# Kernel tuning notes

Measured on AMD Instinct MI355X. Metric: run time of the kernel, lower is better.

Reference implementation:

```python
import jax, jax.numpy as jnp
import numpy as np

N = 50000      # nodes
E = 800000     # edges
C = 128        # dim_feat / channels
D = 256        # dim_dense
OUT = 2        # dim_out
L = 5          # num_layers - 1 GCN2Conv layers
ALPHA = 0.1    # main_param -> GCN2Conv alpha; theta=None -> beta=1.0
SLOPE = 0.01   # LeakyReLU default negative slope


def setup_inputs() -> dict:
    key = jax.random.key(0)
    ks = jax.random.split(key, 6)
    x = jax.random.normal(ks[0], (N, C), jnp.float32)
    edge_index = jax.random.randint(ks[1], (2, E), 0, N, jnp.int32)
    conv_weights = jax.random.normal(ks[2], (L, C, C), jnp.float32) * (1.0 / np.sqrt(C))
    w_dense = jax.random.normal(ks[3], (C, D), jnp.float32) * (1.0 / np.sqrt(C))
    b_dense = jnp.zeros((D,), jnp.float32)
    w_out = jax.random.normal(ks[4], (D, OUT), jnp.float32) * (1.0 / np.sqrt(D))
    b_out = jnp.zeros((OUT,), jnp.float32)
    return dict(x=x, edge_index=edge_index, conv_weights=conv_weights,
                w_dense=w_dense, b_dense=b_dense, w_out=w_out, b_out=b_out)


def _gcn_norm(edge_index, num_nodes):
    """Symmetric gcn_norm with self-loops: returns row, col, D^-1/2 * D^-1/2 edge weights."""
    loop = jnp.arange(num_nodes, dtype=edge_index.dtype)
    row = jnp.concatenate([edge_index[0], loop])  # sources
    col = jnp.concatenate([edge_index[1], loop])  # targets (aggregation index)
    ones = jnp.ones(row.shape[0], jnp.float32)
    deg = jax.ops.segment_sum(ones, col, num_segments=num_nodes)
    dinv = jnp.where(deg > 0, jax.lax.rsqrt(jnp.maximum(deg, 1e-12)), 0.0)
    return row, col, dinv[row] * dinv[col]


def reference(x, edge_index, conv_weights, w_dense, b_dense, w_out, b_out):
    num_nodes = x.shape[0]
    row, col, norm = _gcn_norm(edge_index, num_nodes)
    x0 = x
    for l in range(conv_weights.shape[0]):
        # propagate: h[i] = sum_{j->i} norm * x[j]   (gather -> scatter-add)
        h = jax.ops.segment_sum(norm[:, None] * x[row], col, num_segments=num_nodes)
        # GCN2Conv with shared_weights=True, beta=1 (theta=None): out = ((1-a)h + a*x0) @ W
        out = (1.0 - ALPHA) * h + ALPHA * x0
        x = jax.nn.leaky_relu(out @ conv_weights[l], negative_slope=SLOPE)
    x = x @ w_dense + b_dense
    return x @ w_out + b_out
```

## Files before the change

kernel.cpp:

```cpp
#include <hip/hip_runtime.h>
#include <hip/hip_fp16.h>

#define C 128
#define NOUT 2
#define ALPHA 0.1f
#define SLOPE 0.01f
#define ZP 136

typedef _Float16 half4v __attribute__((ext_vector_type(4)));
typedef float float4v __attribute__((ext_vector_type(4)));


__global__ void count_kernel(const int* __restrict__ col, int* __restrict__ cnt, int E) {
    int e = blockIdx.x * 256 + threadIdx.x;
    if (e < E) atomicAdd(&cnt[col[e]], 1);
}

__global__ __launch_bounds__(1024) void scanA_kernel(const int* __restrict__ cnt,
                                                     int* __restrict__ offs,
                                                     int* __restrict__ bsum,
                                                     float* __restrict__ dinv, int n) {
    __shared__ int wsum[16];
    int t = threadIdx.x, lane = t & 63, wv = t >> 6;
    int i = blockIdx.x * 1024 + t;
    int v = (i < n) ? cnt[i] : 0;
    if (i < n) dinv[i] = rsqrtf((float)(v + 1));
    int sc = v;
    #pragma unroll
    for (int d = 1; d < 64; d <<= 1) {
        int u = __shfl_up(sc, d);
        if (lane >= d) sc += u;
    }
    if (lane == 63) wsum[wv] = sc;
    __syncthreads();
    int woff = 0;
    #pragma unroll
    for (int j = 0; j < 16; ++j) woff += (j < wv) ? wsum[j] : 0;
    if (i < n) offs[i] = woff + sc - v;
    if (t == 0) {
        int tot = 0;
        #pragma unroll
        for (int j = 0; j < 16; ++j) tot += wsum[j];
        bsum[blockIdx.x] = tot;
    }
}

__global__ __launch_bounds__(1024) void scanB_kernel(const int* __restrict__ bsum,
                                                     int* __restrict__ bbase, int nb) {
    __shared__ int wsum[16];
    int t = threadIdx.x, lane = t & 63, wv = t >> 6;
    int v = (t < nb) ? bsum[t] : 0;
    int sc = v;
    #pragma unroll
    for (int d = 1; d < 64; d <<= 1) {
        int u = __shfl_up(sc, d);
        if (lane >= d) sc += u;
    }
    if (lane == 63) wsum[wv] = sc;
    __syncthreads();
    int woff = 0;
    #pragma unroll
    for (int j = 0; j < 16; ++j) woff += (j < wv) ? wsum[j] : 0;
    if (t < nb) bbase[t] = woff + sc - v;
}

__global__ void scanC_kernel(int* __restrict__ offs, int* __restrict__ cursor,
                             const int* __restrict__ bbase, int n, int E) {
    int i = blockIdx.x * 256 + threadIdx.x;
    if (i < n) {
        int o = offs[i] + bbase[i >> 10];
        offs[i] = o;
        cursor[i] = o;
    }
    if (i == n) offs[n] = E;
}

__global__ void fill_kernel(const int* __restrict__ row, const int* __restrict__ col,
                            const float* __restrict__ dinv, int* __restrict__ cursor,
                            unsigned* __restrict__ csr, int E) {
    int base = blockIdx.x * 1024 + threadIdx.x;
    int r[4], c[4];
    bool v[4];
    #pragma unroll
    for (int j = 0; j < 4; ++j) {
        int e = base + j * 256;
        v[j] = e < E;
        r[j] = v[j] ? row[e] : 0;
        c[j] = v[j] ? col[e] : 0;
    }
    float nr[4];
    #pragma unroll
    for (int j = 0; j < 4; ++j) nr[j] = dinv[r[j]] * dinv[c[j]];
    int pos[4];
    #pragma unroll
    for (int j = 0; j < 4; ++j)
        pos[j] = v[j] ? atomicAdd(&cursor[c[j]], 1) : 0;
    #pragma unroll
    for (int j = 0; j < 4; ++j) {
        if (v[j]) {
            union { __half h; unsigned short u; } nh;
            nh.h = __float2half_rn(nr[j]);
            csr[pos[j]] = ((unsigned)r[j] << 16) | (unsigned)nh.u;
        }
    }
}

__global__ __launch_bounds__(256) void convert_kernel(const float* __restrict__ x,
                                                      __half* __restrict__ xh, int n) {
    int g = blockIdx.x * 256 + threadIdx.x;
    if (g >= n * 32) return;
    float4 v = ((const float4*)x)[g];
    union { __half2 h; unsigned u; } a, b;
    a.h = __float22half2_rn(make_float2(v.x, v.y));
    b.h = __float22half2_rn(make_float2(v.z, v.w));
    ((uint2*)xh)[g] = make_uint2(a.u, b.u);
}

__global__ void wtc_kernel(const float* __restrict__ W, _Float16* __restrict__ WT, int total) {
    int idx = blockIdx.x * 256 + threadIdx.x;
    if (idx >= total) return;
    int l = idx >> 14, rem = idx & 16383;
    int nrow = rem >> 7, kk = rem & 127;
    WT[idx] = (_Float16)W[(l << 14) + kk * C + nrow];
}

__global__ void wdc_kernel(const float* __restrict__ wd, _Float16* __restrict__ WDT) {
    int idx = blockIdx.x * 256 + threadIdx.x;
    if (idx >= 256 * C) return;
    int nrow = idx >> 7, kk = idx & 127;
    WDT[idx] = (_Float16)wd[kk * 256 + nrow];
}

__device__ __forceinline__ void accum8(float* a, uint4 q, float w) {
    union { unsigned u; __half2 h; } c;
    float2 f;
    c.u = q.x; f = __half22float2(c.h); a[0] += w * f.x; a[1] += w * f.y;
    c.u = q.y; f = __half22float2(c.h); a[2] += w * f.x; a[3] += w * f.y;
    c.u = q.z; f = __half22float2(c.h); a[4] += w * f.x; a[5] += w * f.y;
    c.u = q.w; f = __half22float2(c.h); a[6] += w * f.x; a[7] += w * f.y;
}

__device__ __forceinline__ uint4 pack8(const float* a) {
    union { __half2 h; unsigned u; } c0, c1, c2, c3;
    c0.h = __float22half2_rn(make_float2(a[0], a[1]));
    c1.h = __float22half2_rn(make_float2(a[2], a[3]));
    c2.h = __float22half2_rn(make_float2(a[4], a[5]));
    c3.h = __float22half2_rn(make_float2(a[6], a[7]));
    return make_uint4(c0.u, c1.u, c2.u, c3.u);
}

__device__ __forceinline__ float norm_of(unsigned m) {
    union { unsigned short u; __half h; } nh;
    nh.u = (unsigned short)(m & 0xffffu);
    return __half2float(nh.h);
}

__global__ __launch_bounds__(256) void agg_kernel(
    const __half* __restrict__ xc, const __half* __restrict__ x0h,
    const int* __restrict__ offs, const unsigned* __restrict__ csr,
    const float* __restrict__ dinv, __half* __restrict__ z, int n)
{
    int node = blockIdx.x * 4 + (threadIdx.x >> 6);
    if (node >= n) return;
    int lane = threadIdx.x & 63;
    int eslot = lane >> 4, cg = lane & 15;
    const uint4* x4 = (const uint4*)xc;
    float a0[8] = {}, a1[8] = {}, a2[8] = {}, a3[8] = {};
    int beg = offs[node], end = offs[node + 1];
    int k = beg + eslot;
    for (; k + 12 < end; k += 16) {
        unsigned m0 = csr[k], m1 = csr[k + 4], m2 = csr[k + 8], m3 = csr[k + 12];
        uint4 q0 = x4[(size_t)(m0 >> 16) * 16 + cg];
        uint4 q1 = x4[(size_t)(m1 >> 16) * 16 + cg];
        uint4 q2 = x4[(size_t)(m2 >> 16) * 16 + cg];
        uint4 q3 = x4[(size_t)(m3 >> 16) * 16 + cg];
        accum8(a0, q0, norm_of(m0));
        accum8(a1, q1, norm_of(m1));
        accum8(a2, q2, norm_of(m2));
        accum8(a3, q3, norm_of(m3));
    }
    for (; k < end; k += 4) {
        unsigned m = csr[k];
        uint4 q = x4[(size_t)(m >> 16) * 16 + cg];
        accum8(a0, q, norm_of(m));
    }
    #pragma unroll
    for (int j = 0; j < 8; ++j) a0[j] += a1[j] + a2[j] + a3[j];
    #pragma unroll
    for (int j = 0; j < 8; ++j) {
        a0[j] += __shfl_xor(a0[j], 16);
        a0[j] += __shfl_xor(a0[j], 32);
    }
    if (eslot == 0) {
        float di = dinv[node], sw = di * di;
        uint4 qs = x4[(size_t)node * 16 + cg];
        accum8(a0, qs, sw);
        uint4 q0x = ((const uint4*)x0h)[(size_t)node * 16 + cg];
        float xr[8] = {};
        accum8(xr, q0x, 1.f);
        float zz[8];
        #pragma unroll
        for (int j = 0; j < 8; ++j) zz[j] = (1.f - ALPHA) * a0[j] + ALPHA * xr[j];
        ((uint4*)z)[(size_t)node * 16 + cg] = pack8(zz);
    }
}

__global__ __launch_bounds__(256) void layer_mfma(
    const __half* __restrict__ zin, const _Float16* __restrict__ WT,
    __half* __restrict__ xn, int n)
{
    __shared__ _Float16 zl[64 * ZP];
    __shared__ _Float16 ol[64 * ZP];
    int i0 = blockIdx.x * 64;
    int t = threadIdx.x;
    int w = t >> 6, lane = t & 63;
    int c = lane & 15, g = lane >> 4;

    const uint4* z4 = (const uint4*)zin;
    for (int p = t; p < 64 * 16; p += 256) {
        int r = p >> 4, c8 = p & 15;
        uint4 zv = make_uint4(0, 0, 0, 0);
        if (i0 + r < n) zv = z4[(size_t)(i0 + r) * 16 + c8];
        *(uint4*)&zl[r * ZP + c8 * 8] = zv;
    }

    half4v bf[8][2];
    #pragma unroll
    for (int kb = 0; kb < 8; ++kb)
        #pragma unroll
        for (int nt = 0; nt < 2; ++nt)
            bf[kb][nt] = *(const half4v*)&WT[((w * 2 + nt) * 16 + c) * C + kb * 16 + 4 * g];

    __syncthreads();

    #pragma unroll
    for (int m = 0; m < 4; ++m) {
        const _Float16* arow = &zl[(m * 16 + c) * ZP];
        half4v af[8];
        #pragma unroll
        for (int kb = 0; kb < 8; ++kb) af[kb] = *(const half4v*)&arow[kb * 16 + 4 * g];
        float4v acc0 = (float4v)0.f, acc1 = (float4v)0.f;
        #pragma unroll
        for (int kb = 0; kb < 8; ++kb) {
            acc0 = __builtin_amdgcn_mfma_f32_16x16x16f16(af[kb], bf[kb][0], acc0, 0, 0, 0);
            acc1 = __builtin_amdgcn_mfma_f32_16x16x16f16(af[kb], bf[kb][1], acc1, 0, 0, 0);
        }
        #pragma unroll
        for (int r = 0; r < 4; ++r) {
            float v0 = acc0[r]; v0 = v0 > 0.f ? v0 : SLOPE * v0;
            float v1 = acc1[r]; v1 = v1 > 0.f ? v1 : SLOPE * v1;
            ol[(m * 16 + 4 * g + r) * ZP + (w * 2 + 0) * 16 + c] = (_Float16)v0;
            ol[(m * 16 + 4 * g + r) * ZP + (w * 2 + 1) * 16 + c] = (_Float16)v1;
        }
    }
    __syncthreads();
    for (int p = t; p < 64 * 16; p += 256) {
        int r = p >> 4, c8 = p & 15;
        int node = i0 + r;
        if (node < n)
            ((uint4*)xn)[(size_t)node * 16 + c8] = *(uint4*)&ol[r * ZP + c8 * 8];
    }
}

__global__ __launch_bounds__(256) void dense_mfma(
    const __half* __restrict__ xin, const _Float16* __restrict__ WDT,
    const float* __restrict__ bd, const float* __restrict__ wo,
    const float* __restrict__ bo, float* __restrict__ out, int n)
{
    __shared__ _Float16 xl[64 * ZP];
    __shared__ float pp[64][4][2];
    int i0 = blockIdx.x * 64;
    int t = threadIdx.x;
    int w = t >> 6, lane = t & 63;
    int c = lane & 15, g = lane >> 4;

    const uint4* g4 = (const uint4*)xin;
    for (int p = t; p < 64 * 16; p += 256) {
        int r = p >> 4, c8 = p & 15;
        uint4 v = make_uint4(0, 0, 0, 0);
        if (i0 + r < n) v = g4[(size_t)(i0 + r) * 16 + c8];
        *(uint4*)&xl[r * ZP + c8 * 8] = v;
    }

    half4v bf[8][4];
    #pragma unroll
    for (int kb = 0; kb < 8; ++kb)
        #pragma unroll
        for (int nt = 0; nt < 4; ++nt)
            bf[kb][nt] = *(const half4v*)&WDT[((w * 4 + nt) * 16 + c) * C + kb * 16 + 4 * g];
    float bdv[4], wo0[4], wo1[4];
    #pragma unroll
    for (int nt = 0; nt < 4; ++nt) {
        int coln = (w * 4 + nt) * 16 + c;
        bdv[nt] = bd[coln];
        wo0[nt] = wo[coln * 2 + 0];
        wo1[nt] = wo[coln * 2 + 1];
    }

    __syncthreads();

    #pragma unroll
    for (int m = 0; m < 4; ++m) {
        const _Float16* arow = &xl[(m * 16 + c) * ZP];
        half4v af[8];
        #pragma unroll
        for (int kb = 0; kb < 8; ++kb) af[kb] = *(const half4v*)&arow[kb * 16 + 4 * g];
        float4v acc[4];
        #pragma unroll
        for (int nt = 0; nt < 4; ++nt) acc[nt] = (float4v)0.f;
        #pragma unroll
        for (int kb = 0; kb < 8; ++kb) {
            #pragma unroll
            for (int nt = 0; nt < 4; ++nt)
                acc[nt] = __builtin_amdgcn_mfma_f32_16x16x16f16(af[kb], bf[kb][nt], acc[nt], 0, 0, 0);
        }
        float p0[4] = {0.f, 0.f, 0.f, 0.f}, p1[4] = {0.f, 0.f, 0.f, 0.f};
        #pragma unroll
        for (int nt = 0; nt < 4; ++nt) {
            #pragma unroll
            for (int r = 0; r < 4; ++r) {
                float hv = acc[nt][r] + bdv[nt];
                p0[r] += hv * wo0[nt];
                p1[r] += hv * wo1[nt];
            }
        }
        #pragma unroll
        for (int ms = 1; ms <= 8; ms <<= 1) {
            #pragma unroll
            for (int r = 0; r < 4; ++r) {
                p0[r] += __shfl_xor(p0[r], ms);
                p1[r] += __shfl_xor(p1[r], ms);
            }
        }
        if (c == 0) {
            #pragma unroll
            for (int r = 0; r < 4; ++r) {
                pp[m * 16 + 4 * g + r][w][0] = p0[r];
                pp[m * 16 + 4 * g + r][w][1] = p1[r];
            }
        }
    }
    __syncthreads();
    if (t < 128) {
        int r = t >> 1, o = t & 1;
        int node = i0 + r;
        if (node < n) {
            float s = pp[r][0][o] + pp[r][1][o] + pp[r][2][o] + pp[r][3][o];
            out[(size_t)node * NOUT + o] = s + bo[o];
        }
    }
}

extern "C" void kernel_launch(void* const* d_in, const int* in_sizes, int n_in,
                              void* d_out, int out_size, void* d_ws, size_t ws_size,
                              hipStream_t stream) {
    const float* x0    = (const float*)d_in[0];
    const int*   ei    = (const int*)d_in[1];
    const float* convW = (const float*)d_in[2];
    const float* wd    = (const float*)d_in[3];
    const float* bd    = (const float*)d_in[4];
    const float* wo    = (const float*)d_in[5];
    const float* bo    = (const float*)d_in[6];
    float* out = (float*)d_out;

    int N = in_sizes[0] / C;
    int E = in_sizes[1] / 2;
    int L = in_sizes[2] / (C * C);
    const int* row = ei;
    const int* col = ei + E;
    int NB = (N + 1023) / 1024;

    char* p = (char*)d_ws;
    auto alloc = [&](size_t bytes) {
        char* r = p;
        p += (bytes + 255) & ~(size_t)255;
        return r;
    };
    int*      cnt    = (int*)alloc((size_t)N * 4);
    int*      offs   = (int*)alloc((size_t)(N + 1) * 4);
    int*      cursor = (int*)alloc((size_t)N * 4);
    int*      bsum   = (int*)alloc((size_t)NB * 4);
    int*      bbase  = (int*)alloc((size_t)NB * 4);
    unsigned* csr    = (unsigned*)alloc((size_t)E * 4);
    float*    dinv   = (float*)alloc((size_t)N * 4);
    __half*   x0h    = (__half*)alloc((size_t)N * C * 2);
    __half*   bufA   = (__half*)alloc((size_t)N * C * 2);
    __half*   zbuf   = (__half*)alloc((size_t)N * C * 2);
    _Float16* WT     = (_Float16*)alloc((size_t)L * C * C * 2);
    _Float16* WDT    = (_Float16*)alloc((size_t)256 * C * 2);

    hipMemsetAsync(cnt, 0, (size_t)N * 4, stream);
    count_kernel<<<(E + 255) / 256, 256, 0, stream>>>(col, cnt, E);
    scanA_kernel<<<NB, 1024, 0, stream>>>(cnt, offs, bsum, dinv, N);
    scanB_kernel<<<1, 1024, 0, stream>>>(bsum, bbase, NB);
    scanC_kernel<<<(N + 256) / 256, 256, 0, stream>>>(offs, cursor, bbase, N, E);
    fill_kernel<<<(E + 1023) / 1024, 256, 0, stream>>>(row, col, dinv, cursor, csr, E);
    convert_kernel<<<(N * 32 + 255) / 256, 256, 0, stream>>>(x0, x0h, N);
    int wtot = L * C * C;
    wtc_kernel<<<(wtot + 255) / 256, 256, 0, stream>>>(convW, WT, wtot);
    wdc_kernel<<<(256 * C + 255) / 256, 256, 0, stream>>>(wd, WDT);

    const __half* xc = x0h;
    for (int l = 0; l < L; ++l) {
        agg_kernel<<<(N + 3) / 4, 256, 0, stream>>>(xc, x0h, offs, csr, dinv, zbuf, N);
        layer_mfma<<<(N + 63) / 64, 256, 0, stream>>>(zbuf, WT + (size_t)l * C * C,
                                                      bufA, N);
        xc = bufA;
    }
    dense_mfma<<<(N + 63) / 64, 256, 0, stream>>>(xc, WDT, bd, wo, bo, out, N);
}
```

Baseline: 411.6 us.

## Record edge ranks during counting to drop fill atomics; half-wave per node in aggregation

The count kernel now stores each edge's atomic rank, so the CSR fill computes positions as offs[col]+rank without a second pass of atomics and without a cursor array. The aggregation kernel assigns 32 lanes per node (two edge slots) instead of 64 (four slots), handles 8 nodes per block, and unrolls 8 gathers per iteration to raise memory-level parallelism for the average degree of about 16. This adds an E-sized rank buffer write and read, and gives each thread more serial edges.

Result: faster. 365.8 us (-11.1%).

```diff
diff --git a/kernel.cpp b/kernel.cpp
--- a/kernel.cpp
+++ b/kernel.cpp
@@ -11,9 +11,10 @@
 typedef float float4v __attribute__((ext_vector_type(4)));
 
 
-__global__ void count_kernel(const int* __restrict__ col, int* __restrict__ cnt, int E) {
+__global__ void count_kernel(const int* __restrict__ col, int* __restrict__ cnt,
+                             int* __restrict__ rank, int E) {
     int e = blockIdx.x * 256 + threadIdx.x;
-    if (e < E) atomicAdd(&cnt[col[e]], 1);
+    if (e < E) rank[e] = atomicAdd(&cnt[col[e]], 1);
 }
 
 __global__ __launch_bounds__(1024) void scanA_kernel(const int* __restrict__ cnt,
@@ -64,43 +65,25 @@
     if (t < nb) bbase[t] = woff + sc - v;
 }
 
-__global__ void scanC_kernel(int* __restrict__ offs, int* __restrict__ cursor,
-                             const int* __restrict__ bbase, int n, int E) {
+__global__ void scanC_kernel(int* __restrict__ offs, const int* __restrict__ bbase,
+                             int n, int E) {
     int i = blockIdx.x * 256 + threadIdx.x;
-    if (i < n) {
-        int o = offs[i] + bbase[i >> 10];
-        offs[i] = o;
-        cursor[i] = o;
-    }
+    if (i < n) offs[i] = offs[i] + bbase[i >> 10];
     if (i == n) offs[n] = E;
 }
 
 __global__ void fill_kernel(const int* __restrict__ row, const int* __restrict__ col,
-                            const float* __restrict__ dinv, int* __restrict__ cursor,
-                            unsigned* __restrict__ csr, int E) {
-    int base = blockIdx.x * 1024 + threadIdx.x;
-    int r[4], c[4];
-    bool v[4];
-    #pragma unroll
-    for (int j = 0; j < 4; ++j) {
+                            const float* __restrict__ dinv, const int* __restrict__ offs,
+                            const int* __restrict__ rank, unsigned* __restrict__ csr, int E) {
+    int base = blockIdx.x * 2048 + threadIdx.x;
+    #pragma unroll
+    for (int j = 0; j < 8; ++j) {
         int e = base + j * 256;
-        v[j] = e < E;
-        r[j] = v[j] ? row[e] : 0;
-        c[j] = v[j] ? col[e] : 0;
-    }
-    float nr[4];
-    #pragma unroll
-    for (int j = 0; j < 4; ++j) nr[j] = dinv[r[j]] * dinv[c[j]];
-    int pos[4];
-    #pragma unroll
-    for (int j = 0; j < 4; ++j)
-        pos[j] = v[j] ? atomicAdd(&cursor[c[j]], 1) : 0;
-    #pragma unroll
-    for (int j = 0; j < 4; ++j) {
-        if (v[j]) {
+        if (e < E) {
+            int r = row[e], c = col[e];
             union { __half h; unsigned short u; } nh;
-            nh.h = __float2half_rn(nr[j]);
-            csr[pos[j]] = ((unsigned)r[j] << 16) | (unsigned)nh.u;
+            nh.h = __float2half_rn(dinv[r] * dinv[c]);
+            csr[offs[c] + rank[e]] = ((unsigned)r << 16) | (unsigned)nh.u;
         }
     }
 }
@@ -160,16 +143,37 @@
     const int* __restrict__ offs, const unsigned* __restrict__ csr,
     const float* __restrict__ dinv, __half* __restrict__ z, int n)
 {
-    int node = blockIdx.x * 4 + (threadIdx.x >> 6);
+    int node = blockIdx.x * 8 + (threadIdx.x >> 5);
     if (node >= n) return;
-    int lane = threadIdx.x & 63;
-    int eslot = lane >> 4, cg = lane & 15;
+    int l32 = threadIdx.x & 31;
+    int sub = l32 >> 4;
+    int cg = l32 & 15;
     const uint4* x4 = (const uint4*)xc;
     float a0[8] = {}, a1[8] = {}, a2[8] = {}, a3[8] = {};
     int beg = offs[node], end = offs[node + 1];
-    int k = beg + eslot;
-    for (; k + 12 < end; k += 16) {
-        unsigned m0 = csr[k], m1 = csr[k + 4], m2 = csr[k + 8], m3 = csr[k + 12];
+    int k = beg + sub;
+    for (; k + 14 < end; k += 16) {
+        unsigned m0 = csr[k], m1 = csr[k + 2], m2 = csr[k + 4], m3 = csr[k + 6];
+        unsigned m4 = csr[k + 8], m5 = csr[k + 10], m6 = csr[k + 12], m7 = csr[k + 14];
+        uint4 q0 = x4[(size_t)(m0 >> 16) * 16 + cg];
+        uint4 q1 = x4[(size_t)(m1 >> 16) * 16 + cg];
+        uint4 q2 = x4[(size_t)(m2 >> 16) * 16 + cg];
+        uint4 q3 = x4[(size_t)(m3 >> 16) * 16 + cg];
+        uint4 q4 = x4[(size_t)(m4 >> 16) * 16 + cg];
+        uint4 q5 = x4[(size_t)(m5 >> 16) * 16 + cg];
+        uint4 q6 = x4[(size_t)(m6 >> 16) * 16 + cg];
+        uint4 q7 = x4[(size_t)(m7 >> 16) * 16 + cg];
+        accum8(a0, q0, norm_of(m0));
+        accum8(a1, q1, norm_of(m1));
+        accum8(a2, q2, norm_of(m2));
+        accum8(a3, q3, norm_of(m3));
+        accum8(a0, q4, norm_of(m4));
+        accum8(a1, q5, norm_of(m5));
+        accum8(a2, q6, norm_of(m6));
+        accum8(a3, q7, norm_of(m7));
+    }
+    for (; k + 6 < end; k += 8) {
+        unsigned m0 = csr[k], m1 = csr[k + 2], m2 = csr[k + 4], m3 = csr[k + 6];
         uint4 q0 = x4[(size_t)(m0 >> 16) * 16 + cg];
         uint4 q1 = x4[(size_t)(m1 >> 16) * 16 + cg];
         uint4 q2 = x4[(size_t)(m2 >> 16) * 16 + cg];
@@ -179,7 +183,7 @@
         accum8(a2, q2, norm_of(m2));
         accum8(a3, q3, norm_of(m3));
     }
-    for (; k < end; k += 4) {
+    for (; k < end; k += 2) {
         unsigned m = csr[k];
         uint4 q = x4[(size_t)(m >> 16) * 16 + cg];
         accum8(a0, q, norm_of(m));
@@ -187,11 +191,8 @@
     #pragma unroll
     for (int j = 0; j < 8; ++j) a0[j] += a1[j] + a2[j] + a3[j];
     #pragma unroll
-    for (int j = 0; j < 8; ++j) {
-        a0[j] += __shfl_xor(a0[j], 16);
-        a0[j] += __shfl_xor(a0[j], 32);
-    }
-    if (eslot == 0) {
+    for (int j = 0; j < 8; ++j) a0[j] += __shfl_xor(a0[j], 16);
+    if (sub == 0) {
         float di = dinv[node], sw = di * di;
         uint4 qs = x4[(size_t)node * 16 + cg];
         accum8(a0, qs, sw);
@@ -378,7 +379,7 @@
     };
     int*      cnt    = (int*)alloc((size_t)N * 4);
     int*      offs   = (int*)alloc((size_t)(N + 1) * 4);
-    int*      cursor = (int*)alloc((size_t)N * 4);
+    int*      rank   = (int*)alloc((size_t)E * 4);
     int*      bsum   = (int*)alloc((size_t)NB * 4);
     int*      bbase  = (int*)alloc((size_t)NB * 4);
     unsigned* csr    = (unsigned*)alloc((size_t)E * 4);
@@ -390,11 +391,11 @@
     _Float16* WDT    = (_Float16*)alloc((size_t)256 * C * 2);
 
     hipMemsetAsync(cnt, 0, (size_t)N * 4, stream);
-    count_kernel<<<(E + 255) / 256, 256, 0, stream>>>(col, cnt, E);
+    count_kernel<<<(E + 255) / 256, 256, 0, stream>>>(col, cnt, rank, E);
     scanA_kernel<<<NB, 1024, 0, stream>>>(cnt, offs, bsum, dinv, N);
     scanB_kernel<<<1, 1024, 0, stream>>>(bsum, bbase, NB);
-    scanC_kernel<<<(N + 256) / 256, 256, 0, stream>>>(offs, cursor, bbase, N, E);
-    fill_kernel<<<(E + 1023) / 1024, 256, 0, stream>>>(row, col, dinv, cursor, csr, E);
+    scanC_kernel<<<(N + 256) / 256, 256, 0, stream>>>(offs, bbase, N, E);
+    fill_kernel<<<(E + 2047) / 2048, 256, 0, stream>>>(row, col, dinv, offs, rank, csr, E);
     convert_kernel<<<(N * 32 + 255) / 256, 256, 0, stream>>>(x0, x0h, N);
     int wtot = L * C * C;
     wtc_kernel<<<(wtot + 255) / 256, 256, 0, stream>>>(convW, WT, wtot);
@@ -402,7 +403,7 @@
 
     const __half* xc = x0h;
     for (int l = 0; l < L; ++l) {
-        agg_kernel<<<(N + 3) / 4, 256, 0, stream>>>(xc, x0h, offs, csr, dinv, zbuf, N);
+        agg_kernel<<<(N + 7) / 8, 256, 0, stream>>>(xc, x0h, offs, csr, dinv, zbuf, N);
         layer_mfma<<<(N + 63) / 64, 256, 0, stream>>>(zbuf, WT + (size_t)l * C * C,
                                                       bufA, N);
         xc = bufA;
```
